# Performance work log

Hardware: AMD Instinct MI355X
Metric: run time of the kernel (lower is better)

Reference implementation:

```python
import jax, jax.numpy as jnp
import numpy as np

B, N, C, E = 8, 4096, 128, 131072  # batch, nodes, channels (in==out), edges


def _linear_params(key, fan_in, fan_out):
    kw, kb = jax.random.split(key)
    s = 1.0 / np.sqrt(fan_in).astype(np.float32)
    W = jax.random.uniform(kw, (fan_in, fan_out), jnp.float32, -s, s)
    b = jax.random.uniform(kb, (fan_out,), jnp.float32, -s, s)
    return W, b


def setup_inputs() -> dict:
    key = jax.random.key(0)
    ks = jax.random.split(key, 6)
    x = jax.random.normal(ks[0], (B, N, C), jnp.float32)
    edge_index = jax.random.randint(ks[1], (2, E), 0, N, jnp.int64)
    W0, b0 = _linear_params(ks[2], C, C)        # lin0: in -> out
    W1, b1 = _linear_params(ks[3], 2 * C, C)    # lin1: 2*out -> out
    W2, b2 = _linear_params(ks[4], C, C)        # lin2: out -> out
    Wo, bo = _linear_params(ks[5], C, C)        # output: out -> out
    return {"x": x, "edge_index": edge_index, "W0": W0, "b0": b0,
            "W1": W1, "b1": b1, "W2": W2, "b2": b2, "Wo": Wo, "bo": bo}


def reference(x, edge_index, W0, b0, W1, b1, W2, b2, Wo, bo):
    n = x.shape[1]
    # symmetric 0/1 adjacency (duplicate edges collapse via .set), zero diagonal
    adj = jnp.zeros((n, n), x.dtype)
    adj = adj.at[edge_index[0], edge_index[1]].set(1.0)
    adj = adj.at[edge_index[1], edge_index[0]].set(1.0)
    diag = jnp.arange(n)
    adj = adj.at[diag, diag].set(0.0)
    h = x @ W0 + b0                               # [B, N, C]
    agg = jnp.einsum('ij,bjd->bid', adj, h)       # neighbor aggregation
    cat = jnp.concatenate([x, agg], axis=-1)      # [B, N, 2C]
    out = (cat @ W1 + b1) @ W2 + b2
    out = jax.nn.gelu(out, approximate=False) @ Wo + bo  # torch exact GELU
    return x + out
```

## Files before the change

kernel.cpp:

```cpp
#include <hip/hip_runtime.h>
#include <hip/hip_bf16.h>
#include <math.h>

#define NN 4096
#define BB 8
#define CC 128
#define EE 131072
#define M_ROWS (BB*NN)
#define DEG_CAP 512

typedef __attribute__((ext_vector_type(8))) short short8;
typedef __attribute__((ext_vector_type(4))) float f32x4;

__device__ __forceinline__ float bf2f(unsigned int u){
    union { unsigned int i; float f; } v; v.i = u << 16; return v.f;
}
__device__ __forceinline__ unsigned short f2bf(float f){
    union { float f; unsigned int i; } v; v.f = f;
    unsigned int u = v.i;
    unsigned int r = u + 0x7FFFu + ((u >> 16) & 1u);
    return (unsigned short)(r >> 16);
}

__device__ __forceinline__ int swz(int r, int k2 ){
    return r * 256 + (k2 ^ ((r & 7) << 4));
}

__global__ __launch_bounds__(256) void k_prep_w(const float* __restrict__ W0, const float* __restrict__ W1,
                                                const float* __restrict__ W2, const float* __restrict__ Wo,
                                                unsigned short* __restrict__ Wt0, unsigned short* __restrict__ Wt1a,
                                                unsigned short* __restrict__ Wt1b, unsigned short* __restrict__ Wt2,
                                                unsigned short* __restrict__ Wto){
    int idx = blockIdx.x * blockDim.x + threadIdx.x;
    int s = idx >> 14;
    int e = idx & 16383;
    int n = e >> 7, k = e & 127;
    float v; unsigned short* dst;
    switch (s){
        case 0:  v = W0[k*128+n];        dst = Wt0;  break;
        case 1:  v = W1[k*128+n];        dst = Wt1a; break;
        case 2:  v = W1[(128+k)*128+n];  dst = Wt1b; break;
        case 3:  v = W2[k*128+n];        dst = Wt2;  break;
        default: v = Wo[k*128+n];        dst = Wto;  break;
    }
    dst[n*128+k] = f2bf(v);
}

__global__ __launch_bounds__(256) void k_scatter(const int* __restrict__ ei,
                                                 unsigned int* __restrict__ bits){
    int e = blockIdx.x * blockDim.x + threadIdx.x;
    if (e < EE){
        int u = ei[e], v = ei[EE + e];
        atomicOr(&bits[u * 128 + (v >> 5)], 1u << (v & 31));
        atomicOr(&bits[v * 128 + (u >> 5)], 1u << (u & 31));
    }
}

__global__ __launch_bounds__(128) void k_csr(const unsigned int* __restrict__ bits,
                                             int* __restrict__ cols, int* __restrict__ deg){
    __shared__ int sc[128];
    int i = blockIdx.x, t = threadIdx.x;
    unsigned int w = bits[i * 128 + t];
    if (t == (i >> 5)) w &= ~(1u << (i & 31));
    int c = __popc(w);
    sc[t] = c; __syncthreads();
    int val = c;
    for (int off = 1; off < 128; off <<= 1){
        int add = (t >= off) ? sc[t - off] : 0;
        __syncthreads();
        val += add; sc[t] = val;
        __syncthreads();
    }
    int total = sc[127];
    int pos = val - c;
    unsigned int ww = w;
    while (ww){
        int b = __ffs(ww) - 1;
        ww &= ww - 1;
        if (pos < DEG_CAP) cols[(size_t)i * DEG_CAP + pos] = t * 32 + b;
        pos++;
    }
    if (t == 0) deg[i] = total < DEG_CAP ? total : DEG_CAP;
}

__device__ __forceinline__ void acc8(uint4 u, float* a){
    a[0] += bf2f(u.x & 0xFFFFu); a[1] += bf2f(u.x >> 16);
    a[2] += bf2f(u.y & 0xFFFFu); a[3] += bf2f(u.y >> 16);
    a[4] += bf2f(u.z & 0xFFFFu); a[5] += bf2f(u.z >> 16);
    a[6] += bf2f(u.w & 0xFFFFu); a[7] += bf2f(u.w >> 16);
}

__global__ __launch_bounds__(256) void k_agg(const unsigned short* __restrict__ hT,
                                             const int* __restrict__ cols,
                                             const int* __restrict__ deg,
                                             unsigned short* __restrict__ aggbf){
    __shared__ int scol[DEG_CAP];
    __shared__ float red[128][9];
    const int i = blockIdx.x, t = threadIdx.x;
    const int half = t >> 7, lane = t & 127;
    const int d = deg[i];
    const int* cl = cols + (size_t)i * DEG_CAP;
    for (int q = t; q < d; q += 256) scol[q] = cl[q];
    __syncthreads();

    const unsigned short* hp = hT + lane * 8;
    float a[8];
    #pragma unroll
    for (int c = 0; c < 8; c++) a[c] = 0.f;

    int n = half;
    for (; n + 6 < d; n += 8){
        int j0 = scol[n], j1 = scol[n+2], j2 = scol[n+4], j3 = scol[n+6];
        uint4 u0 = *((const uint4*)(hp + ((size_t)j0 << 10)));
        uint4 u1 = *((const uint4*)(hp + ((size_t)j1 << 10)));
        uint4 u2 = *((const uint4*)(hp + ((size_t)j2 << 10)));
        uint4 u3 = *((const uint4*)(hp + ((size_t)j3 << 10)));
        acc8(u0, a); acc8(u1, a); acc8(u2, a); acc8(u3, a);
    }
    for (; n < d; n += 2){
        uint4 u0 = *((const uint4*)(hp + ((size_t)scol[n] << 10)));
        acc8(u0, a);
    }

    if (half){
        #pragma unroll
        for (int c = 0; c < 8; c++) red[lane][c] = a[c];
    }
    __syncthreads();
    if (!half){
        #pragma unroll
        for (int c = 0; c < 8; c++) a[c] += red[lane][c];
        int b  = lane >> 4;
        int ch = (lane * 8) & 127;
        uint4 o;
        o.x = (unsigned)f2bf(a[0]) | ((unsigned)f2bf(a[1]) << 16);
        o.y = (unsigned)f2bf(a[2]) | ((unsigned)f2bf(a[3]) << 16);
        o.z = (unsigned)f2bf(a[4]) | ((unsigned)f2bf(a[5]) << 16);
        o.w = (unsigned)f2bf(a[6]) | ((unsigned)f2bf(a[7]) << 16);
        *((uint4*)(aggbf + (size_t)b * (NN*128) + (size_t)i * 128 + ch)) = o;
    }
}

__device__ __forceinline__ void stage_a_bf16(const unsigned short* __restrict__ src, int blockRow,
                                             unsigned short* As, int t){
    #pragma unroll
    for (int it = 0; it < 4; ++it){
        int g = it * 2048 + t * 8;
        int r = g >> 7, k = g & 127;
        uint4 v = *((const uint4*)(src + (size_t)(blockRow + r) * 128 + k));
        *((uint4*)((char*)As + swz(r, k * 2))) = v;
    }
}
__device__ __forceinline__ void stage_a_f32(const float* __restrict__ src, int blockRow,
                                            unsigned short* As, int t){
    #pragma unroll
    for (int it = 0; it < 4; ++it){
        int g = it * 2048 + t * 8;
        int r = g >> 7, k = g & 127;
        const float* p = src + (size_t)(blockRow + r) * 128 + k;
        float4 lo = *((const float4*)p);
        float4 hi = *((const float4*)(p + 4));
        ushort4 w0, w1;
        w0.x = f2bf(lo.x); w0.y = f2bf(lo.y); w0.z = f2bf(lo.z); w0.w = f2bf(lo.w);
        w1.x = f2bf(hi.x); w1.y = f2bf(hi.y); w1.z = f2bf(hi.z); w1.w = f2bf(hi.w);
        char* dst = (char*)As + swz(r, k * 2);
        *((ushort4*)dst) = w0;
        *((ushort4*)(dst + 8)) = w1;
    }
}
__device__ __forceinline__ void stage_w(const unsigned short* __restrict__ Wt,
                                        unsigned short* Ws, int t){
    #pragma unroll
    for (int it = 0; it < 8; ++it){
        int g = it * 2048 + t * 8;
        int r = g >> 7, k = g & 127;
        uint4 v = *((const uint4*)(Wt + r * 128 + k));
        *((uint4*)((char*)Ws + swz(r, k * 2))) = v;
    }
}
__device__ __forceinline__ void mfma_pass(const unsigned short* As, const unsigned short* Ws,
                                          int wr, int wc, int l15, int lh, f32x4 acc[2][4]){
    #pragma unroll
    for (int ks = 0; ks < 4; ++ks){
        const int kc = ks * 32 + lh * 8;
        short8 af[2], bfv[4];
        #pragma unroll
        for (int m = 0; m < 2; m++){
            int r = wr + m * 16 + l15;
            af[m] = *((const short8*)((const char*)As + swz(r, kc * 2)));
        }
        #pragma unroll
        for (int n = 0; n < 4; n++){
            int r = wc + n * 16 + l15;
            bfv[n] = *((const short8*)((const char*)Ws + swz(r, kc * 2)));
        }
        #pragma unroll
        for (int m = 0; m < 2; m++)
            #pragma unroll
            for (int n = 0; n < 4; n++)
                acc[m][n] = __builtin_amdgcn_mfma_f32_16x16x32_bf16(af[m], bfv[n], acc[m][n], 0, 0, 0);
    }
}

__global__ __launch_bounds__(256) void k_gemm0(const float* __restrict__ x,
                                               const unsigned short* __restrict__ Wt0,
                                               const float* __restrict__ b0,
                                               unsigned short* __restrict__ hT){
    __shared__ unsigned short As[64*128];
    __shared__ unsigned short Ws[128*128];
    const int t = threadIdx.x;
    const int blockRow = blockIdx.x * 64;
    stage_a_f32(x, blockRow, As, t);
    stage_w(Wt0, Ws, t);
    __syncthreads();
    const int lane = t & 63, w = t >> 6;
    const int wr = (w >> 1) * 32, wc = (w & 1) * 64;
    const int l15 = lane & 15, lh = lane >> 4;
    f32x4 acc[2][4];
    #pragma unroll
    for (int m = 0; m < 2; m++) for (int n = 0; n < 4; n++) acc[m][n] = (f32x4)(0.0f);
    mfma_pass(As, Ws, wr, wc, l15, lh, acc);
    #pragma unroll
    for (int m = 0; m < 2; m++){
        #pragma unroll
        for (int rr = 0; rr < 4; rr++){
            int row = blockRow + wr + m * 16 + lh * 4 + rr;
            int b_ = row >> 12, j = row & 4095;
            #pragma unroll
            for (int n = 0; n < 4; n++){
                int col = wc + n * 16 + l15;
                float v = acc[m][n][rr] + b0[col];
                hT[(size_t)j * 1024 + b_ * 128 + col] = f2bf(v);
            }
        }
    }
}

__global__ __launch_bounds__(256) void k_gemm1(const float* __restrict__ x,
                                               const unsigned short* __restrict__ agg,
                                               const unsigned short* __restrict__ Wt1a,
                                               const unsigned short* __restrict__ Wt1b,
                                               const float* __restrict__ b1,
                                               unsigned short* __restrict__ t1bf){
    __shared__ unsigned short As[64*128];
    __shared__ unsigned short Ws[128*128];
    const int t = threadIdx.x;
    const int blockRow = blockIdx.x * 64;
    const int lane = t & 63, w = t >> 6;
    const int wr = (w >> 1) * 32, wc = (w & 1) * 64;
    const int l15 = lane & 15, lh = lane >> 4;
    f32x4 acc[2][4];
    #pragma unroll
    for (int m = 0; m < 2; m++) for (int n = 0; n < 4; n++) acc[m][n] = (f32x4)(0.0f);

    stage_a_f32(x, blockRow, As, t);
    stage_w(Wt1a, Ws, t);
    __syncthreads();
    mfma_pass(As, Ws, wr, wc, l15, lh, acc);
    __syncthreads();
    stage_a_bf16(agg, blockRow, As, t);
    stage_w(Wt1b, Ws, t);
    __syncthreads();
    mfma_pass(As, Ws, wr, wc, l15, lh, acc);

    #pragma unroll
    for (int m = 0; m < 2; m++){
        #pragma unroll
        for (int rr = 0; rr < 4; rr++){
            int row = blockRow + wr + m * 16 + lh * 4 + rr;
            #pragma unroll
            for (int n = 0; n < 4; n++){
                int col = wc + n * 16 + l15;
                float v = acc[m][n][rr] + b1[col];
                t1bf[(size_t)row * 128 + col] = f2bf(v);
            }
        }
    }
}

__global__ __launch_bounds__(256) void k_gemm23(const unsigned short* __restrict__ t1bf,
                                                const unsigned short* __restrict__ Wt2,
                                                const unsigned short* __restrict__ Wto,
                                                const float* __restrict__ b2,
                                                const float* __restrict__ bo,
                                                const float* __restrict__ x,
                                                float* __restrict__ out){
    __shared__ unsigned short As[64*128];
    __shared__ unsigned short Ws2[128*128];
    __shared__ unsigned short Wso[128*128];
    const int t = threadIdx.x;
    const int blockRow = blockIdx.x * 64;
    const int lane = t & 63, w = t >> 6;
    const int wr = (w >> 1) * 32, wc = (w & 1) * 64;
    const int l15 = lane & 15, lh = lane >> 4;

    stage_a_bf16(t1bf, blockRow, As, t);
    stage_w(Wt2, Ws2, t);
    stage_w(Wto, Wso, t);
    __syncthreads();

    f32x4 acc[2][4];
    #pragma unroll
    for (int m = 0; m < 2; m++) for (int n = 0; n < 4; n++) acc[m][n] = (f32x4)(0.0f);
    mfma_pass(As, Ws2, wr, wc, l15, lh, acc);
    __syncthreads();

    #pragma unroll
    for (int m = 0; m < 2; m++){
        #pragma unroll
        for (int rr = 0; rr < 4; rr++){
            int rl = wr + m * 16 + lh * 4 + rr;
            #pragma unroll
            for (int n = 0; n < 4; n++){
                int col = wc + n * 16 + l15;
                float v = acc[m][n][rr] + b2[col];
                v = 0.5f * v * (1.0f + erff(v * 0.70710678118f));
                *((unsigned short*)((char*)As + swz(rl, col * 2))) = f2bf(v);
            }
        }
    }
    __syncthreads();

    f32x4 acc2[2][4];
    #pragma unroll
    for (int m = 0; m < 2; m++) for (int n = 0; n < 4; n++) acc2[m][n] = (f32x4)(0.0f);
    mfma_pass(As, Wso, wr, wc, l15, lh, acc2);

    #pragma unroll
    for (int m = 0; m < 2; m++){
        #pragma unroll
        for (int rr = 0; rr < 4; rr++){
            int row = blockRow + wr + m * 16 + lh * 4 + rr;
            #pragma unroll
            for (int n = 0; n < 4; n++){
                int col = wc + n * 16 + l15;
                float v = acc2[m][n][rr] + bo[col] + x[(size_t)row * 128 + col];
                out[(size_t)row * 128 + col] = v;
            }
        }
    }
}

extern "C" void kernel_launch(void* const* d_in, const int* in_sizes, int n_in,
                              void* d_out, int out_size, void* d_ws, size_t ws_size,
                              hipStream_t stream) {
    const float* x  = (const float*)d_in[0];
    const int*   ei = (const int*)d_in[1];
    const float* W0 = (const float*)d_in[2];
    const float* b0 = (const float*)d_in[3];
    const float* W1 = (const float*)d_in[4];
    const float* b1 = (const float*)d_in[5];
    const float* W2 = (const float*)d_in[6];
    const float* b2 = (const float*)d_in[7];
    const float* Wo = (const float*)d_in[8];
    const float* bo = (const float*)d_in[9];
    float* out = (float*)d_out;

    char* ws = (char*)d_ws;
    unsigned int* bits   = (unsigned int*)(ws + 0);
    int*   cols          = (int*)(ws + 2097152);
    int*   deg           = (int*)(ws + 10485760);
    unsigned short* hT   = (unsigned short*)(ws + 10502144);
    unsigned short* aggb = (unsigned short*)(ws + 18890752);
    unsigned short* t1bf = (unsigned short*)(ws + 27279360);
    unsigned short* Wt0  = (unsigned short*)(ws + 35667968);
    unsigned short* Wt1a = (unsigned short*)(ws + 35667968 + 32768);
    unsigned short* Wt1b = (unsigned short*)(ws + 35667968 + 65536);
    unsigned short* Wt2  = (unsigned short*)(ws + 35667968 + 98304);
    unsigned short* Wto  = (unsigned short*)(ws + 35667968 + 131072);

    hipMemsetAsync(bits, 0, 2097152, stream);

    k_prep_w<<<320, 256, 0, stream>>>(W0, W1, W2, Wo, Wt0, Wt1a, Wt1b, Wt2, Wto);
    k_scatter<<<EE / 256, 256, 0, stream>>>(ei, bits);
    k_csr<<<NN, 128, 0, stream>>>(bits, cols, deg);

    k_gemm0<<<M_ROWS / 64, 256, 0, stream>>>(x, Wt0, b0, hT);
    k_agg<<<NN, 256, 0, stream>>>(hT, cols, deg, aggb);
    k_gemm1<<<M_ROWS / 64, 256, 0, stream>>>(x, aggb, Wt1a, Wt1b, b1, t1bf);
    k_gemm23<<<M_ROWS / 64, 256, 0, stream>>>(t1bf, Wt2, Wto, b2, bo, x, out);
}
```

Baseline: 93.37 us.

## Use batch-major h layout with wave-per-node aggregation and fuse bitmap clear into init

The h buffer switches from node-major (all batches per node, interleaved) to plain batch-major row layout. The aggregation kernel now assigns one wave per (batch, node) pair: each lane gathers 4 bytes from a 256-byte neighbor row, with no block-wide sync or cross-half reduction. The bitmap memset is folded into the weight-prep kernel, which removes one launch. The trade-off is smaller per-lane gathers and reading the column list once per batch instead of once per node, in exchange for more parallelism and a simpler GEMM0 store pattern.

```diff
diff --git a/kernel.cpp b/kernel.cpp
--- a/kernel.cpp
+++ b/kernel.cpp
@@ -26,12 +26,18 @@
     return r * 256 + (k2 ^ ((r & 7) << 4));
 }
 
-__global__ __launch_bounds__(256) void k_prep_w(const float* __restrict__ W0, const float* __restrict__ W1,
-                                                const float* __restrict__ W2, const float* __restrict__ Wo,
-                                                unsigned short* __restrict__ Wt0, unsigned short* __restrict__ Wt1a,
-                                                unsigned short* __restrict__ Wt1b, unsigned short* __restrict__ Wt2,
-                                                unsigned short* __restrict__ Wto){
-    int idx = blockIdx.x * blockDim.x + threadIdx.x;
+__global__ __launch_bounds__(256) void k_init(uint4* __restrict__ bits4,
+                                              const float* __restrict__ W0, const float* __restrict__ W1,
+                                              const float* __restrict__ W2, const float* __restrict__ Wo,
+                                              unsigned short* __restrict__ Wt0, unsigned short* __restrict__ Wt1a,
+                                              unsigned short* __restrict__ Wt1b, unsigned short* __restrict__ Wt2,
+                                              unsigned short* __restrict__ Wto){
+    int bid = blockIdx.x, t = threadIdx.x;
+    if (bid < 512){
+        bits4[bid * 256 + t] = (uint4){0u, 0u, 0u, 0u};
+        return;
+    }
+    int idx = (bid - 512) * 256 + t;
     int s = idx >> 14;
     int e = idx & 16383;
     int n = e >> 7, k = e & 127;
@@ -83,62 +89,38 @@
     if (t == 0) deg[i] = total < DEG_CAP ? total : DEG_CAP;
 }
 
-__device__ __forceinline__ void acc8(uint4 u, float* a){
-    a[0] += bf2f(u.x & 0xFFFFu); a[1] += bf2f(u.x >> 16);
-    a[2] += bf2f(u.y & 0xFFFFu); a[3] += bf2f(u.y >> 16);
-    a[4] += bf2f(u.z & 0xFFFFu); a[5] += bf2f(u.z >> 16);
-    a[6] += bf2f(u.w & 0xFFFFu); a[7] += bf2f(u.w >> 16);
-}
-
-__global__ __launch_bounds__(256) void k_agg(const unsigned short* __restrict__ hT,
+__global__ __launch_bounds__(256) void k_agg(const unsigned short* __restrict__ h,
                                              const int* __restrict__ cols,
                                              const int* __restrict__ deg,
-                                             unsigned short* __restrict__ aggbf){
-    __shared__ int scol[DEG_CAP];
-    __shared__ float red[128][9];
-    const int i = blockIdx.x, t = threadIdx.x;
-    const int half = t >> 7, lane = t & 127;
+                                             unsigned short* __restrict__ agg){
+    __shared__ int scol[4][DEG_CAP];
+    const int t = threadIdx.x;
+    const int w = t >> 6, lane = t & 63;
+    const int b = blockIdx.x >> 10;
+    const int i = ((blockIdx.x & 1023) << 2) + w;
     const int d = deg[i];
     const int* cl = cols + (size_t)i * DEG_CAP;
-    for (int q = t; q < d; q += 256) scol[q] = cl[q];
-    __syncthreads();
-
-    const unsigned short* hp = hT + lane * 8;
-    float a[8];
-    #pragma unroll
-    for (int c = 0; c < 8; c++) a[c] = 0.f;
-
-    int n = half;
-    for (; n + 6 < d; n += 8){
-        int j0 = scol[n], j1 = scol[n+2], j2 = scol[n+4], j3 = scol[n+6];
-        uint4 u0 = *((const uint4*)(hp + ((size_t)j0 << 10)));
-        uint4 u1 = *((const uint4*)(hp + ((size_t)j1 << 10)));
-        uint4 u2 = *((const uint4*)(hp + ((size_t)j2 << 10)));
-        uint4 u3 = *((const uint4*)(hp + ((size_t)j3 << 10)));
-        acc8(u0, a); acc8(u1, a); acc8(u2, a); acc8(u3, a);
-    }
-    for (; n < d; n += 2){
-        uint4 u0 = *((const uint4*)(hp + ((size_t)scol[n] << 10)));
-        acc8(u0, a);
-    }
-
-    if (half){
-        #pragma unroll
-        for (int c = 0; c < 8; c++) red[lane][c] = a[c];
-    }
-    __syncthreads();
-    if (!half){
-        #pragma unroll
-        for (int c = 0; c < 8; c++) a[c] += red[lane][c];
-        int b  = lane >> 4;
-        int ch = (lane * 8) & 127;
-        uint4 o;
-        o.x = (unsigned)f2bf(a[0]) | ((unsigned)f2bf(a[1]) << 16);
-        o.y = (unsigned)f2bf(a[2]) | ((unsigned)f2bf(a[3]) << 16);
-        o.z = (unsigned)f2bf(a[4]) | ((unsigned)f2bf(a[5]) << 16);
-        o.w = (unsigned)f2bf(a[6]) | ((unsigned)f2bf(a[7]) << 16);
-        *((uint4*)(aggbf + (size_t)b * (NN*128) + (size_t)i * 128 + ch)) = o;
-    }
+    for (int q = lane; q < d; q += 64) scol[w][q] = cl[q];
+
+    const unsigned short* hb = h + (size_t)b * (NN*128) + lane * 2;
+    float a0 = 0.f, a1 = 0.f;
+    int n = 0;
+    for (; n + 3 < d; n += 4){
+        int j0 = scol[w][n], j1 = scol[w][n+1], j2 = scol[w][n+2], j3 = scol[w][n+3];
+        unsigned int u0 = *((const unsigned int*)(hb + ((size_t)j0 << 7)));
+        unsigned int u1 = *((const unsigned int*)(hb + ((size_t)j1 << 7)));
+        unsigned int u2 = *((const unsigned int*)(hb + ((size_t)j2 << 7)));
+        unsigned int u3 = *((const unsigned int*)(hb + ((size_t)j3 << 7)));
+        a0 += bf2f(u0 & 0xFFFFu) + bf2f(u1 & 0xFFFFu) + bf2f(u2 & 0xFFFFu) + bf2f(u3 & 0xFFFFu);
+        a1 += bf2f(u0 >> 16)     + bf2f(u1 >> 16)     + bf2f(u2 >> 16)     + bf2f(u3 >> 16);
+    }
+    for (; n < d; ++n){
+        unsigned int u0 = *((const unsigned int*)(hb + ((size_t)scol[w][n] << 7)));
+        a0 += bf2f(u0 & 0xFFFFu);
+        a1 += bf2f(u0 >> 16);
+    }
+    unsigned int o = (unsigned)f2bf(a0) | ((unsigned)f2bf(a1) << 16);
+    *((unsigned int*)(agg + (size_t)b * (NN*128) + ((size_t)i << 7) + lane * 2)) = o;
 }
 
 __device__ __forceinline__ void stage_a_bf16(const unsigned short* __restrict__ src, int blockRow,
@@ -205,7 +187,7 @@
 __global__ __launch_bounds__(256) void k_gemm0(const float* __restrict__ x,
                                                const unsigned short* __restrict__ Wt0,
                                                const float* __restrict__ b0,
-                                               unsigned short* __restrict__ hT){
+                                               unsigned short* __restrict__ h){
     __shared__ unsigned short As[64*128];
     __shared__ unsigned short Ws[128*128];
     const int t = threadIdx.x;
@@ -225,12 +207,11 @@
         #pragma unroll
         for (int rr = 0; rr < 4; rr++){
             int row = blockRow + wr + m * 16 + lh * 4 + rr;
-            int b_ = row >> 12, j = row & 4095;
             #pragma unroll
             for (int n = 0; n < 4; n++){
                 int col = wc + n * 16 + l15;
                 float v = acc[m][n][rr] + b0[col];
-                hT[(size_t)j * 1024 + b_ * 128 + col] = f2bf(v);
+                h[(size_t)row * 128 + col] = f2bf(v);
             }
         }
     }
@@ -360,7 +341,7 @@
     unsigned int* bits   = (unsigned int*)(ws + 0);
     int*   cols          = (int*)(ws + 2097152);
     int*   deg           = (int*)(ws + 10485760);
-    unsigned short* hT   = (unsigned short*)(ws + 10502144);
+    unsigned short* h    = (unsigned short*)(ws + 10502144);
     unsigned short* aggb = (unsigned short*)(ws + 18890752);
     unsigned short* t1bf = (unsigned short*)(ws + 27279360);
     unsigned short* Wt0  = (unsigned short*)(ws + 35667968);
@@ -369,14 +350,12 @@
     unsigned short* Wt2  = (unsigned short*)(ws + 35667968 + 98304);
     unsigned short* Wto  = (unsigned short*)(ws + 35667968 + 131072);
 
-    hipMemsetAsync(bits, 0, 2097152, stream);
-
-    k_prep_w<<<320, 256, 0, stream>>>(W0, W1, W2, Wo, Wt0, Wt1a, Wt1b, Wt2, Wto);
+    k_init<<<832, 256, 0, stream>>>((uint4*)bits, W0, W1, W2, Wo, Wt0, Wt1a, Wt1b, Wt2, Wto);
     k_scatter<<<EE / 256, 256, 0, stream>>>(ei, bits);
     k_csr<<<NN, 128, 0, stream>>>(bits, cols, deg);
 
-    k_gemm0<<<M_ROWS / 64, 256, 0, stream>>>(x, Wt0, b0, hT);
-    k_agg<<<NN, 256, 0, stream>>>(hT, cols, deg, aggb);
+    k_gemm0<<<M_ROWS / 64, 256, 0, stream>>>(x, Wt0, b0, h);
+    k_agg<<<BB * (NN / 4), 256, 0, stream>>>(h, cols, deg, aggb);
     k_gemm1<<<M_ROWS / 64, 256, 0, stream>>>(x, aggb, Wt1a, Wt1b, b1, t1bf);
     k_gemm23<<<M_ROWS / 64, 256, 0, stream>>>(t1bf, Wt2, Wto, b2, bo, x, out);
 }
```

Result: faster. 80.68 us (-13.6%).
